# Optimization experiments

Measured on AMD Instinct MI355X. Metric: run time of the kernel, lower is better.

Reference implementation:

```python
import jax, jax.numpy as jnp
import numpy as np

NH = 16            # num_heads
HD = 64            # head_dim
HID = NH * HD      # hidden_size = 1024
MLP = 4 * HID      # mlp_hidden_dim = 4096
B, LI, LT = 1, 2048, 512
EPS = 1e-6


def _ln(x):
    # LayerNorm without affine, eps=1e-6
    mu = jnp.mean(x, -1, keepdims=True)
    var = jnp.mean((x - mu) ** 2, -1, keepdims=True)
    return (x - mu) * jax.lax.rsqrt(var + EPS)


def _rms(x, scale):
    # QK RMSNorm over head_dim with learned scale
    return x * jax.lax.rsqrt(jnp.mean(x * x, -1, keepdims=True) + EPS) * scale


def _modulate(vec, w, b):
    # Modulation(double=True): Linear(silu(vec)) -> 6 chunks, broadcast over seq
    out = jnp.dot(jax.nn.silu(vec), w) + b           # [B, 6*HID]
    return jnp.split(out[:, None, :], 6, axis=-1)


def _qkv(x_mod, qkv_w, q_scale, k_scale):
    b, l, _ = x_mod.shape
    qkv = jnp.dot(x_mod, qkv_w).reshape(b, l, 3, NH, HD)
    qkv = jnp.transpose(qkv, (2, 0, 3, 1, 4))         # [3, B, H, L, D]
    q, k, v = qkv[0], qkv[1], qkv[2]
    return _rms(q, q_scale), _rms(k, k_scale), v


def _attn(q, k, v):
    s = jnp.einsum('bhqd,bhkd->bhqk', q, k) * (HD ** -0.5)
    a = jax.nn.softmax(s, axis=-1)
    o = jnp.einsum('bhqk,bhkd->bhqd', a, v)
    b, h, l, d = o.shape
    return jnp.transpose(o, (0, 2, 1, 3)).reshape(b, l, h * d)  # B L (H D)


def _mlp(x, w1, b1, w2, b2):
    return jnp.dot(jax.nn.gelu(jnp.dot(x, w1) + b1, approximate=True), w2) + b2


def setup_inputs() -> dict:
    key = jax.random.key(0)
    ks = iter(jax.random.split(key, 40))
    def rn(shape, s=1.0):
        return jax.random.normal(next(ks), shape, jnp.float32) * s
    return {
        'img': rn((B, LI, HID)),
        'txt': rn((B, LT, HID)),
        'vec': rn((B, HID)),
        'img_mod_w': rn((HID, 6 * HID), 0.02), 'img_mod_b': jnp.zeros((6 * HID,), jnp.float32),
        'txt_mod_w': rn((HID, 6 * HID), 0.02), 'txt_mod_b': jnp.zeros((6 * HID,), jnp.float32),
        'img_qkv_w': rn((HID, 3 * HID), 0.02),
        'img_q_scale': jnp.ones((HD,), jnp.float32), 'img_k_scale': jnp.ones((HD,), jnp.float32),
        'img_proj_w': rn((HID, HID), 0.02), 'img_proj_b': jnp.zeros((HID,), jnp.float32),
        'img_mlp_w1': rn((HID, MLP), 0.02), 'img_mlp_b1': jnp.zeros((MLP,), jnp.float32),
        'img_mlp_w2': rn((MLP, HID), 0.02), 'img_mlp_b2': jnp.zeros((HID,), jnp.float32),
        'txt_qkv_w': rn((HID, 3 * HID), 0.02),
        'txt_q_scale': jnp.ones((HD,), jnp.float32), 'txt_k_scale': jnp.ones((HD,), jnp.float32),
        'txt_proj_w': rn((HID, HID), 0.02), 'txt_proj_b': jnp.zeros((HID,), jnp.float32),
        'txt_mlp_w1': rn((HID, MLP), 0.02), 'txt_mlp_b1': jnp.zeros((MLP,), jnp.float32),
        'txt_mlp_w2': rn((MLP, HID), 0.02), 'txt_mlp_b2': jnp.zeros((HID,), jnp.float32),
    }


def reference(img, txt, vec,
              img_mod_w, img_mod_b, txt_mod_w, txt_mod_b,
              img_qkv_w, img_q_scale, img_k_scale, img_proj_w, img_proj_b,
              img_mlp_w1, img_mlp_b1, img_mlp_w2, img_mlp_b2,
              txt_qkv_w, txt_q_scale, txt_k_scale, txt_proj_w, txt_proj_b,
              txt_mlp_w1, txt_mlp_b1, txt_mlp_w2, txt_mlp_b2):
    i_sh1, i_sc1, i_g1, i_sh2, i_sc2, i_g2 = _modulate(vec, img_mod_w, img_mod_b)
    t_sh1, t_sc1, t_g1, t_sh2, t_sc2, t_g2 = _modulate(vec, txt_mod_w, txt_mod_b)
    iq, ik, iv = _qkv((1 + i_sc1) * _ln(img) + i_sh1, img_qkv_w, img_q_scale, img_k_scale)
    tq, tk, tv = _qkv((1 + t_sc1) * _ln(txt) + t_sh1, txt_qkv_w, txt_q_scale, txt_k_scale)
    q = jnp.concatenate((tq, iq), axis=2)   # txt tokens first, as in source
    k = jnp.concatenate((tk, ik), axis=2)
    v = jnp.concatenate((tv, iv), axis=2)
    attn = _attn(q, k, v)                    # [B, LT+LI, HID]
    lt = txt.shape[1]
    txt_a, img_a = attn[:, :lt], attn[:, lt:]
    img = img + i_g1 * (jnp.dot(img_a, img_proj_w) + img_proj_b)
    img = img + i_g2 * _mlp((1 + i_sc2) * _ln(img) + i_sh2, img_mlp_w1, img_mlp_b1, img_mlp_w2, img_mlp_b2)
    txt = txt + t_g1 * (jnp.dot(txt_a, txt_proj_w) + txt_proj_b)
    txt = txt + t_g2 * _mlp((1 + t_sc2) * _ln(txt) + t_sh2, txt_mlp_w1, txt_mlp_b1, txt_mlp_w2, txt_mlp_b2)
    return (img, txt)
```

## Files before the change

### kernel.cpp

```cpp
#include <hip/hip_runtime.h>
#include <hip/hip_bf16.h>
#include <stdint.h>


#define NHEAD 16
#define HDIM  64
#define HIDD  1024
#define MLPD  4096
#define L_IMG 2048
#define L_TXT 512
#define L_TOT 2560
#define EPSV  1e-6f
#define LOG2E 1.44269504088896f

typedef __attribute__((ext_vector_type(8))) __bf16 bf16x8;
typedef __attribute__((ext_vector_type(4))) float  f32x4;

__device__ __forceinline__ float u2f(uint16_t u) {
    uint32_t i = (uint32_t)u << 16;
    float f; __builtin_memcpy(&f, &i, 4);
    return f;
}
__device__ __forceinline__ uint16_t f2u(float f) {
    uint32_t i; __builtin_memcpy(&i, &f, 4);
    uint32_t r = (i + 0x7fffu + ((i >> 16) & 1u)) >> 16;
    return (uint16_t)r;
}
__device__ __forceinline__ uint32_t pk2(float a, float b) {
    __hip_bfloat162 h = __float22bfloat162_rn(float2{a, b});
    uint32_t r; __builtin_memcpy(&r, &h, 4);
    return r;
}
__device__ __forceinline__ float gelu_tanh(float x) {
    float x3 = x * x * x;
    float t  = tanhf(0.7978845608028654f * (x + 0.044715f * x3));
    return 0.5f * x * (1.f + t);
}

__global__ __launch_bounds__(256) void transpose_all_kernel(
        const float* __restrict__ i0, const float* __restrict__ i1,
        const float* __restrict__ i2, const float* __restrict__ i3,
        const float* __restrict__ i4, const float* __restrict__ i5,
        const float* __restrict__ i6, const float* __restrict__ i7,
        uint16_t* __restrict__ o0, uint16_t* __restrict__ o1,
        uint16_t* __restrict__ o2, uint16_t* __restrict__ o3,
        uint16_t* __restrict__ o4, uint16_t* __restrict__ o5,
        uint16_t* __restrict__ o6, uint16_t* __restrict__ o7) {
    __shared__ float tile[64][65];
    const int b = blockIdx.x, t = threadIdx.x;
    const float* in; uint16_t* out; int K, N, rel;
    if      (b < 768)  { in = i0; out = o0; K = 1024; N = 3072; rel = b; }
    else if (b < 1536) { in = i1; out = o1; K = 1024; N = 3072; rel = b - 768; }
    else if (b < 1792) { in = i2; out = o2; K = 1024; N = 1024; rel = b - 1536; }
    else if (b < 2048) { in = i3; out = o3; K = 1024; N = 1024; rel = b - 1792; }
    else if (b < 3072) { in = i4; out = o4; K = 1024; N = 4096; rel = b - 2048; }
    else if (b < 4096) { in = i5; out = o5; K = 1024; N = 4096; rel = b - 3072; }
    else if (b < 5120) { in = i6; out = o6; K = 4096; N = 1024; rel = b - 4096; }
    else               { in = i7; out = o7; K = 4096; N = 1024; rel = b - 5120; }
    const int nx = N >> 6;
    const int c0 = (rel % nx) * 64;
    const int r0 = (rel / nx) * 64;
#pragma unroll
    for (int p = 0; p < 4; p++) {
        int row  = p * 16 + (t >> 4);
        int col4 = (t & 15) * 4;
        float4 v = *(const float4*)(in + (size_t)(r0 + row) * N + c0 + col4);
        tile[row][col4 + 0] = v.x; tile[row][col4 + 1] = v.y;
        tile[row][col4 + 2] = v.z; tile[row][col4 + 3] = v.w;
    }
    __syncthreads();
#pragma unroll
    for (int p = 0; p < 4; p++) {
        int row  = p * 16 + (t >> 4);
        int col4 = (t & 15) * 4;
        ushort4 v;
        v.x = f2u(tile[col4 + 0][row]); v.y = f2u(tile[col4 + 1][row]);
        v.z = f2u(tile[col4 + 2][row]); v.w = f2u(tile[col4 + 3][row]);
        *(ushort4*)(out + (size_t)(c0 + row) * K + r0 + col4) = v;
    }
}

__global__ __launch_bounds__(256) void transpose_v_kernel(const uint16_t* __restrict__ Vb,
                                                          uint16_t* __restrict__ Vt) {
    __shared__ uint16_t tile[64][68];
    const int t  = threadIdx.x;
    const int p0 = blockIdx.x * 64;
    const int h  = blockIdx.y;
    const uint16_t* src = Vb + ((size_t)h * L_TOT + p0) * HDIM;
#pragma unroll
    for (int p = 0; p < 4; p++) {
        int row = p * 16 + (t >> 4);
        int c4  = (t & 15) * 4;
        ushort4 v = *(const ushort4*)(src + (size_t)row * HDIM + c4);
        tile[row][c4 + 0] = v.x; tile[row][c4 + 1] = v.y;
        tile[row][c4 + 2] = v.z; tile[row][c4 + 3] = v.w;
    }
    __syncthreads();
    uint16_t* dst = Vt + (size_t)h * HDIM * L_TOT;
#pragma unroll
    for (int p = 0; p < 4; p++) {
        int d  = p * 16 + (t >> 4);
        int c4 = (t & 15) * 4;
        ushort4 v;
        v.x = tile[c4 + 0][d]; v.y = tile[c4 + 1][d];
        v.z = tile[c4 + 2][d]; v.w = tile[c4 + 3][d];
        *(ushort4*)(dst + (size_t)d * L_TOT + p0 + c4) = v;
    }
}

__global__ __launch_bounds__(256) void mod_gemv_kernel(const float* __restrict__ vec,
                                                       const float* __restrict__ w0,
                                                       const float* __restrict__ b0,
                                                       float* __restrict__ m0,
                                                       const float* __restrict__ w1,
                                                       const float* __restrict__ b1,
                                                       float* __restrict__ m1) {
    const float* w   = blockIdx.z ? w1 : w0;
    const float* b   = blockIdx.z ? b1 : b0;
    float*       mod = blockIdx.z ? m1 : m0;
    __shared__ float s[HIDD];
    __shared__ float part[4][64];
    const int t = threadIdx.x;
    for (int i = t; i < HIDD; i += 256) {
        float x = vec[i];
        s[i] = x / (1.f + __expf(-x));
    }
    __syncthreads();
    const int col = blockIdx.x * 64 + (t & 63);
    const int ks  = t >> 6;
    float acc = 0.f;
#pragma unroll 8
    for (int k = ks * 256; k < ks * 256 + 256; k++)
        acc += s[k] * w[(size_t)k * 6144 + col];
    part[ks][t & 63] = acc;
    __syncthreads();
    if (t < 64) {
        float r = part[0][t] + part[1][t] + part[2][t] + part[3][t];
        mod[blockIdx.x * 64 + t] = r + b[blockIdx.x * 64 + t];
    }
}

__global__ __launch_bounds__(256) void ln_mod_kernel(const float* __restrict__ xi,
                                                     const float* __restrict__ xt,
                                                     const float* __restrict__ mi,
                                                     const float* __restrict__ mt_,
                                                     int scOff, int shOff,
                                                     uint16_t* __restrict__ oi,
                                                     uint16_t* __restrict__ ot) {
    __shared__ float red[8];
    int row = blockIdx.x;
    const float* x; const float* mod; uint16_t* xm;
    if (row < L_IMG) { x = xi; mod = mi; xm = oi; }
    else             { x = xt; mod = mt_; xm = ot; row -= L_IMG; }
    const int t = threadIdx.x;
    const size_t base = (size_t)row * HIDD + t * 4;
    float4 u = *(const float4*)(x + base);
    float v[4] = {u.x, u.y, u.z, u.w};
    float s = v[0] + v[1] + v[2] + v[3];
    float q = v[0]*v[0] + v[1]*v[1] + v[2]*v[2] + v[3]*v[3];
#pragma unroll
    for (int o = 32; o; o >>= 1) { s += __shfl_down(s, o); q += __shfl_down(q, o); }
    if ((t & 63) == 0) { red[t >> 6] = s; red[4 + (t >> 6)] = q; }
    __syncthreads();
    s = red[0] + red[1] + red[2] + red[3];
    q = red[4] + red[5] + red[6] + red[7];
    const float mu  = s * (1.f / HIDD);
    const float var = q * (1.f / HIDD) - mu * mu;
    const float rs  = rsqrtf(var + EPSV);
    ushort4 o;
    {
        int col = t * 4;
        float y0 = (v[0] - mu) * rs, y1 = (v[1] - mu) * rs;
        float y2 = (v[2] - mu) * rs, y3 = (v[3] - mu) * rs;
        o.x = f2u(y0 + mod[scOff + col + 0] * y0 + mod[shOff + col + 0]);
        o.y = f2u(y1 + mod[scOff + col + 1] * y1 + mod[shOff + col + 1]);
        o.z = f2u(y2 + mod[scOff + col + 2] * y2 + mod[shOff + col + 2]);
        o.w = f2u(y3 + mod[scOff + col + 3] * y3 + mod[shOff + col + 3]);
    }
    *(ushort4*)(xm + base) = o;
}

template <int EPI>
__global__ __launch_bounds__(256, 2) void gemm_kernel(
        const uint16_t* __restrict__ A0, const uint16_t* __restrict__ A1,
        const uint16_t* __restrict__ B0, const uint16_t* __restrict__ B1,
        int M0, int M1, int N, int K,
        const float* __restrict__ bias0, const float* __restrict__ bias1,
        const float* __restrict__ gate0, const float* __restrict__ gate1,
        const float* __restrict__ resid0, const float* __restrict__ resid1,
        void* __restrict__ C0, void* __restrict__ C1) {
    const int z = blockIdx.z;
    const int M = z ? M1 : M0;
    const int m0 = blockIdx.y * 128;
    if (m0 >= M) return;
    const uint16_t* A     = z ? A1 : A0;
    const uint16_t* BT    = z ? B1 : B0;
    const float*    bias  = z ? bias1 : bias0;
    const float*    gate  = z ? gate1 : gate0;
    const float*    resid = z ? resid1 : resid0;
    void*           C     = z ? C1 : C0;

    __shared__ uint16_t As[2][128 * 32];
    __shared__ uint16_t Bs[2][128 * 32];
    const int t = threadIdx.x;
    const int w = t >> 6, l = t & 63;
    const int lr = l & 15, lg = l >> 4;
    const int n0 = blockIdx.x * 128;
    const int srow = l >> 2, scol = (l & 3) * 8;
    const int c0 = w * 2;
    const int wr = (w >> 1) * 64, wc = (w & 1) * 64;

    auto stage = [&](int buf, int kt) {
#pragma unroll
        for (int i = 0; i < 2; i++) {
            const int c = c0 + i;
            const uint16_t* ga = A  + (size_t)(m0 + c * 16 + srow) * K + kt + scol;
            const uint16_t* gb = BT + (size_t)(n0 + c * 16 + srow) * K + kt + scol;
            __builtin_amdgcn_global_load_lds(
                (__attribute__((address_space(1))) void*)ga,
                (__attribute__((address_space(3))) void*)(As[buf] + c * 512), 16, 0, 0);
            __builtin_amdgcn_global_load_lds(
                (__attribute__((address_space(1))) void*)gb,
                (__attribute__((address_space(3))) void*)(Bs[buf] + c * 512), 16, 0, 0);
        }
    };

    const f32x4 z4 = {0.f, 0.f, 0.f, 0.f};
    f32x4 acc[4][4];
#pragma unroll
    for (int i = 0; i < 4; i++)
#pragma unroll
        for (int j = 0; j < 4; j++) acc[i][j] = z4;

    stage(0, 0);
    int cur = 0;
    for (int kt = 0; kt < K; kt += 32) {
        __syncthreads();
        if (kt + 32 < K) stage(cur ^ 1, kt + 32);
        bf16x8 af[4], bfr[4];
#pragma unroll
        for (int mi = 0; mi < 4; mi++)
            af[mi] = *(const bf16x8*)(As[cur] + (wr + mi * 16 + lr) * 32 + lg * 8);
#pragma unroll
        for (int nj = 0; nj < 4; nj++)
            bfr[nj] = *(const bf16x8*)(Bs[cur] + (wc + nj * 16 + lr) * 32 + lg * 8);
#pragma unroll
        for (int mi = 0; mi < 4; mi++)
#pragma unroll
            for (int nj = 0; nj < 4; nj++)
                acc[mi][nj] = __builtin_amdgcn_mfma_f32_16x16x32_bf16(
                    af[mi], bfr[nj], acc[mi][nj], 0, 0, 0);
        cur ^= 1;
    }

#pragma unroll
    for (int mi = 0; mi < 4; mi++)
#pragma unroll
        for (int nj = 0; nj < 4; nj++) {
            const int col = n0 + wc + nj * 16 + lr;
            float bv = 0.f, gv = 0.f;
            if (EPI != 0) bv = bias[col];
            if (EPI == 2) gv = gate[col];
#pragma unroll
            for (int j = 0; j < 4; j++) {
                const int row = m0 + wr + mi * 16 + lg * 4 + j;
                const size_t idx = (size_t)row * N + col;
                float v = acc[mi][nj][j];
                if (EPI == 0) {
                    ((uint16_t*)C)[idx] = f2u(v);
                } else if (EPI == 1) {
                    ((uint16_t*)C)[idx] = f2u(gelu_tanh(v + bv));
                } else {
                    ((float*)C)[idx] = resid[idx] + gv * (v + bv);
                }
            }
        }
}

__global__ __launch_bounds__(256, 2) void gemm_splitk_kernel(
        const uint16_t* __restrict__ A0, const uint16_t* __restrict__ A1,
        const uint16_t* __restrict__ B0, const uint16_t* __restrict__ B1,
        int M0, int M1, int N, int K, int KS,
        float* __restrict__ P0, float* __restrict__ P1) {
    const int z = blockIdx.z & 1;
    const int split = blockIdx.z >> 1;
    const int M = z ? M1 : M0;
    const int m0 = blockIdx.y * 128;
    if (m0 >= M) return;
    const uint16_t* A  = z ? A1 : A0;
    const uint16_t* BT = z ? B1 : B0;
    float* P = (z ? P1 : P0) + (size_t)split * M * N;

    __shared__ uint16_t As[2][128 * 32];
    __shared__ uint16_t Bs[2][128 * 32];
    const int t = threadIdx.x;
    const int w = t >> 6, l = t & 63;
    const int lr = l & 15, lg = l >> 4;
    const int n0 = blockIdx.x * 128;
    const int srow = l >> 2, scol = (l & 3) * 8;
    const int c0 = w * 2;
    const int wr = (w >> 1) * 64, wc = (w & 1) * 64;

    auto stage = [&](int buf, int kt) {
#pragma unroll
        for (int i = 0; i < 2; i++) {
            const int c = c0 + i;
            const uint16_t* ga = A  + (size_t)(m0 + c * 16 + srow) * K + kt + scol;
            const uint16_t* gb = BT + (size_t)(n0 + c * 16 + srow) * K + kt + scol;
            __builtin_amdgcn_global_load_lds(
                (__attribute__((address_space(1))) void*)ga,
                (__attribute__((address_space(3))) void*)(As[buf] + c * 512), 16, 0, 0);
            __builtin_amdgcn_global_load_lds(
                (__attribute__((address_space(1))) void*)gb,
                (__attribute__((address_space(3))) void*)(Bs[buf] + c * 512), 16, 0, 0);
        }
    };

    const f32x4 z4 = {0.f, 0.f, 0.f, 0.f};
    f32x4 acc[4][4];
#pragma unroll
    for (int i = 0; i < 4; i++)
#pragma unroll
        for (int j = 0; j < 4; j++) acc[i][j] = z4;

    const int kbeg = split * KS, kend = kbeg + KS;
    stage(0, kbeg);
    int cur = 0;
    for (int kt = kbeg; kt < kend; kt += 32) {
        __syncthreads();
        if (kt + 32 < kend) stage(cur ^ 1, kt + 32);
        bf16x8 af[4], bfr[4];
#pragma unroll
        for (int mi = 0; mi < 4; mi++)
            af[mi] = *(const bf16x8*)(As[cur] + (wr + mi * 16 + lr) * 32 + lg * 8);
#pragma unroll
        for (int nj = 0; nj < 4; nj++)
            bfr[nj] = *(const bf16x8*)(Bs[cur] + (wc + nj * 16 + lr) * 32 + lg * 8);
#pragma unroll
        for (int mi = 0; mi < 4; mi++)
#pragma unroll
            for (int nj = 0; nj < 4; nj++)
                acc[mi][nj] = __builtin_amdgcn_mfma_f32_16x16x32_bf16(
                    af[mi], bfr[nj], acc[mi][nj], 0, 0, 0);
        cur ^= 1;
    }

#pragma unroll
    for (int mi = 0; mi < 4; mi++)
#pragma unroll
        for (int nj = 0; nj < 4; nj++) {
            const int col = n0 + wc + nj * 16 + lr;
#pragma unroll
            for (int j = 0; j < 4; j++) {
                const int row = m0 + wr + mi * 16 + lg * 4 + j;
                P[(size_t)row * N + col] = acc[mi][nj][j];
            }
        }
}

template <int NS>
__global__ __launch_bounds__(256) void splitk_reduce_kernel(
        const float* __restrict__ P0, const float* __restrict__ P1,
        const float* __restrict__ bias0, const float* __restrict__ bias1,
        const float* __restrict__ gate0, const float* __restrict__ gate1,
        const float* __restrict__ resid0, const float* __restrict__ resid1,
        float* __restrict__ O0, float* __restrict__ O1, int M0, int M1) {
    const int z = blockIdx.z;
    const float* P     = z ? P1 : P0;
    const float* bias  = z ? bias1 : bias0;
    const float* gate  = z ? gate1 : gate0;
    const float* resid = z ? resid1 : resid0;
    float*       O     = z ? O1 : O0;
    const int M = z ? M1 : M0;
    const size_t MN = (size_t)M * HIDD;
    const size_t nvec = MN / 4;
    for (size_t i = blockIdx.x * 256 + threadIdx.x; i < nvec; i += (size_t)gridDim.x * 256) {
        const size_t e = i * 4;
        const int col = (int)(e & (HIDD - 1));
        float4 bi = *(const float4*)(bias + col);
        float sx = bi.x, sy = bi.y, sz = bi.z, sw = bi.w;
#pragma unroll
        for (int sp = 0; sp < NS; sp++) {
            float4 a = *(const float4*)(P + (size_t)sp * MN + e);
            sx += a.x; sy += a.y; sz += a.z; sw += a.w;
        }
        float4 r = *(const float4*)(resid + e);
        float4 g = *(const float4*)(gate + col);
        float4 o;
        o.x = r.x + g.x * sx;
        o.y = r.y + g.y * sy;
        o.z = r.z + g.z * sz;
        o.w = r.w + g.w * sw;
        *(float4*)(O + e) = o;
    }
}

__global__ __launch_bounds__(256) void rms_scatter_kernel(
        const uint16_t* __restrict__ qkvi, const uint16_t* __restrict__ qkvt,
        const float* __restrict__ iqs, const float* __restrict__ iks,
        const float* __restrict__ tqs, const float* __restrict__ tks,
        uint16_t* __restrict__ Q, uint16_t* __restrict__ Kb, uint16_t* __restrict__ V) {
    const int p = blockIdx.x;
    const uint16_t* base;
    const float* qs; const float* ks;
    if (p < L_TXT) { base = qkvt + (size_t)p * 3072;            qs = tqs; ks = tks; }
    else           { base = qkvi + (size_t)(p - L_TXT) * 3072;  qs = iqs; ks = iks; }
    const int t = threadIdx.x;
    const int head = t >> 4, d0 = (t & 15) * 4;
    const size_t obase = ((size_t)head * L_TOT + p) * HDIM + d0;
    {
        ushort4 u = *(const ushort4*)(base + head * HDIM + d0);
        float v0 = u2f(u.x), v1 = u2f(u.y), v2 = u2f(u.z), v3 = u2f(u.w);
        float ss = v0*v0 + v1*v1 + v2*v2 + v3*v3;
        ss += __shfl_xor(ss, 1); ss += __shfl_xor(ss, 2);
        ss += __shfl_xor(ss, 4); ss += __shfl_xor(ss, 8);
        float inv = rsqrtf(ss * (1.f / HDIM) + EPSV) * (0.125f * LOG2E);
        ushort4 o;
        o.x = f2u(v0 * inv * qs[d0 + 0]);
        o.y = f2u(v1 * inv * qs[d0 + 1]);
        o.z = f2u(v2 * inv * qs[d0 + 2]);
        o.w = f2u(v3 * inv * qs[d0 + 3]);
        *(ushort4*)(Q + obase) = o;
    }
    {
        ushort4 u = *(const ushort4*)(base + HIDD + head * HDIM + d0);
        float v0 = u2f(u.x), v1 = u2f(u.y), v2 = u2f(u.z), v3 = u2f(u.w);
        float ss = v0*v0 + v1*v1 + v2*v2 + v3*v3;
        ss += __shfl_xor(ss, 1); ss += __shfl_xor(ss, 2);
        ss += __shfl_xor(ss, 4); ss += __shfl_xor(ss, 8);
        float inv = rsqrtf(ss * (1.f / HDIM) + EPSV);
        ushort4 o;
        o.x = f2u(v0 * inv * ks[d0 + 0]);
        o.y = f2u(v1 * inv * ks[d0 + 1]);
        o.z = f2u(v2 * inv * ks[d0 + 2]);
        o.w = f2u(v3 * inv * ks[d0 + 3]);
        *(ushort4*)(Kb + obase) = o;
    }
    {
        ushort4 u = *(const ushort4*)(base + 2 * HIDD + head * HDIM + d0);
        *(ushort4*)(V + obase) = u;
    }
}

__global__ __launch_bounds__(256, 4) void attn_kernel(const uint16_t* __restrict__ Q,
                                                      const uint16_t* __restrict__ Kg,
                                                      const uint16_t* __restrict__ Vt,
                                                      uint16_t* __restrict__ Opart,
                                                      float* __restrict__ lbuf) {
    __shared__ __align__(16) uint16_t Ks[64 * 64];
    __shared__ __align__(16) uint16_t Vs[64 * 64];
    __shared__ __align__(16) uint16_t Pl[4][16][72];
    const int t = threadIdx.x;
    const int w = t >> 6, l = t & 63;
    const int lr = l & 15, lg = l >> 4;
    const int h = blockIdx.y;
    const int s = blockIdx.z;
    const int q0 = blockIdx.x * 64 + w * 16;
    const uint16_t* Qh = Q  + (size_t)h * L_TOT * HDIM;
    const uint16_t* Kh = Kg + (size_t)h * L_TOT * HDIM;
    const uint16_t* Vh = Vt + (size_t)h * HDIM * L_TOT;

    const bf16x8 qf0 = *(const bf16x8*)(Qh + (size_t)(q0 + lr) * HDIM + lg * 8);
    const bf16x8 qf1 = *(const bf16x8*)(Qh + (size_t)(q0 + lr) * HDIM + 32 + lg * 8);

    const int rl = l >> 3;
    const int ce = ((l & 7) ^ rl) * 8;
    const int r0 = w * 16 + rl;
    const int r1 = r0 + 8;
    const int sw = lr & 7;

    const f32x4 z4 = {0.f, 0.f, 0.f, 0.f};
    f32x4 of[4] = {z4, z4, z4, z4};
    float lsum = 0.f;

    const int kbeg = s * (L_TOT / 2);
    const uint16_t* kS0 = Kh + (size_t)(kbeg + r0) * HDIM + ce;
    const uint16_t* kS1 = Kh + (size_t)(kbeg + r1) * HDIM + ce;
    const uint16_t* vS0 = Vh + (size_t)r0 * L_TOT + kbeg + ce;
    const uint16_t* vS1 = Vh + (size_t)r1 * L_TOT + kbeg + ce;

    for (int it = 0; it < (L_TOT / 2) / 64; ++it) {
        __syncthreads();
        __builtin_amdgcn_global_load_lds(
            (__attribute__((address_space(1))) void*)kS0,
            (__attribute__((address_space(3))) void*)(Ks + w * 1024), 16, 0, 0);
        __builtin_amdgcn_global_load_lds(
            (__attribute__((address_space(1))) void*)kS1,
            (__attribute__((address_space(3))) void*)(Ks + w * 1024 + 512), 16, 0, 0);
        __builtin_amdgcn_global_load_lds(
            (__attribute__((address_space(1))) void*)vS0,
            (__attribute__((address_space(3))) void*)(Vs + w * 1024), 16, 0, 0);
        __builtin_amdgcn_global_load_lds(
            (__attribute__((address_space(1))) void*)vS1,
            (__attribute__((address_space(3))) void*)(Vs + w * 1024 + 512), 16, 0, 0);
        kS0 += (size_t)64 * HDIM; kS1 += (size_t)64 * HDIM;
        vS0 += 64; vS1 += 64;
        __syncthreads();
        f32x4 sf[4] = {z4, z4, z4, z4};
#pragma unroll
        for (int kb = 0; kb < 4; kb++) {
            bf16x8 a0 = *(const bf16x8*)(Ks + (kb * 16 + lr) * 64 + ((lg ^ sw) * 8));
            bf16x8 a1 = *(const bf16x8*)(Ks + (kb * 16 + lr) * 64 + (((4 + lg) ^ sw) * 8));
            sf[kb] = __builtin_amdgcn_mfma_f32_16x16x32_bf16(a0, qf0, sf[kb], 0, 0, 0);
            sf[kb] = __builtin_amdgcn_mfma_f32_16x16x32_bf16(a1, qf1, sf[kb], 0, 0, 0);
        }
        uint32_t pw[8];
        float rs = 0.f;
#pragma unroll
        for (int kb = 0; kb < 4; kb++) {
            float p0 = exp2f(sf[kb][0]);
            float p1 = exp2f(sf[kb][1]);
            float p2 = exp2f(sf[kb][2]);
            float p3 = exp2f(sf[kb][3]);
            rs += (p0 + p1) + (p2 + p3);
            pw[kb * 2]     = pk2(p0, p1);
            pw[kb * 2 + 1] = pk2(p2, p3);
        }
        lsum += rs;
#pragma unroll
        for (int kb = 0; kb < 4; kb++) {
            uint2 u = {pw[kb * 2], pw[kb * 2 + 1]};
            *(uint2*)&Pl[w][lr][kb * 16 + lg * 4] = u;
        }
        bf16x8 pb0 = *(const bf16x8*)&Pl[w][lr][lg * 8];
        bf16x8 pb1 = *(const bf16x8*)&Pl[w][lr][32 + lg * 8];
#pragma unroll
        for (int dj = 0; dj < 4; dj++) {
            bf16x8 v0 = *(const bf16x8*)(Vs + (dj * 16 + lr) * 64 + ((lg ^ sw) * 8));
            bf16x8 v1 = *(const bf16x8*)(Vs + (dj * 16 + lr) * 64 + (((4 + lg) ^ sw) * 8));
            of[dj] = __builtin_amdgcn_mfma_f32_16x16x32_bf16(v0, pb0, of[dj], 0, 0, 0);
            of[dj] = __builtin_amdgcn_mfma_f32_16x16x32_bf16(v1, pb1, of[dj], 0, 0, 0);
        }
    }
    lsum += __shfl_xor(lsum, 16);
    lsum += __shfl_xor(lsum, 32);
    const float inv = 1.f / lsum;
    const int row = q0 + lr;
    const size_t ob = ((size_t)(s * NHEAD + h) * L_TOT + row) * HDIM;
#pragma unroll
    for (int dj = 0; dj < 4; dj++) {
        uint2 u;
        u.x = pk2(of[dj][0] * inv, of[dj][1] * inv);
        u.y = pk2(of[dj][2] * inv, of[dj][3] * inv);
        *(uint2*)(Opart + ob + dj * 16 + lg * 4) = u;
    }
    if (lg == 0) lbuf[(size_t)(s * NHEAD + h) * L_TOT + row] = lsum;
}

__global__ __launch_bounds__(256) void attn_merge_kernel(const uint16_t* __restrict__ Opart,
                                                         const float* __restrict__ lbuf,
                                                         uint16_t* __restrict__ attn) {
    const int t = threadIdx.x;
    const int row = blockIdx.x * 16 + (t >> 4);
    const int h = blockIdx.y;
    const int d = (t & 15) * 4;
    const size_t i0 = (size_t)(0 * NHEAD + h) * L_TOT + row;
    const size_t i1 = (size_t)(1 * NHEAD + h) * L_TOT + row;
    float l0 = lbuf[i0], l1 = lbuf[i1];
    float inv = 1.f / (l0 + l1);
    float w0 = l0 * inv, w1 = l1 * inv;
    ushort4 a = *(const ushort4*)(Opart + i0 * HDIM + d);
    ushort4 b = *(const ushort4*)(Opart + i1 * HDIM + d);
    ushort4 o;
    o.x = f2u(u2f(a.x) * w0 + u2f(b.x) * w1);
    o.y = f2u(u2f(a.y) * w0 + u2f(b.y) * w1);
    o.z = f2u(u2f(a.z) * w0 + u2f(b.z) * w1);
    o.w = f2u(u2f(a.w) * w0 + u2f(b.w) * w1);
    *(ushort4*)(attn + (size_t)row * HIDD + h * HDIM + d) = o;
}

extern "C" void kernel_launch(void* const* d_in, const int* in_sizes, int n_in,
                              void* d_out, int out_size, void* d_ws, size_t ws_size,
                              hipStream_t stream) {
    const float* img        = (const float*)d_in[0];
    const float* txt        = (const float*)d_in[1];
    const float* vec        = (const float*)d_in[2];
    const float* img_mod_w  = (const float*)d_in[3];
    const float* img_mod_b  = (const float*)d_in[4];
    const float* txt_mod_w  = (const float*)d_in[5];
    const float* txt_mod_b  = (const float*)d_in[6];
    const float* img_qkv_w  = (const float*)d_in[7];
    const float* img_q_s    = (const float*)d_in[8];
    const float* img_k_s    = (const float*)d_in[9];
    const float* img_proj_w = (const float*)d_in[10];
    const float* img_proj_b = (const float*)d_in[11];
    const float* img_mlp_w1 = (const float*)d_in[12];
    const float* img_mlp_b1 = (const float*)d_in[13];
    const float* img_mlp_w2 = (const float*)d_in[14];
    const float* img_mlp_b2 = (const float*)d_in[15];
    const float* txt_qkv_w  = (const float*)d_in[16];
    const float* txt_q_s    = (const float*)d_in[17];
    const float* txt_k_s    = (const float*)d_in[18];
    const float* txt_proj_w = (const float*)d_in[19];
    const float* txt_proj_b = (const float*)d_in[20];
    const float* txt_mlp_w1 = (const float*)d_in[21];
    const float* txt_mlp_b1 = (const float*)d_in[22];
    const float* txt_mlp_w2 = (const float*)d_in[23];
    const float* txt_mlp_b2 = (const float*)d_in[24];

    float* out_img = (float*)d_out;
    float* out_txt = out_img + (size_t)L_IMG * HIDD;

    char* ws = (char*)d_ws;
    size_t off = 0;
    auto alloc = [&](size_t bytes) -> void* {
        void* p = ws + off;
        off += bytes;
        off = (off + 255) & ~(size_t)255;
        return p;
    };
    uint16_t* wtQKVi = (uint16_t*)alloc((size_t)3072 * 1024 * 2);
    uint16_t* wtQKVt = (uint16_t*)alloc((size_t)3072 * 1024 * 2);
    uint16_t* wtPRJi = (uint16_t*)alloc((size_t)1024 * 1024 * 2);
    uint16_t* wtPRJt = (uint16_t*)alloc((size_t)1024 * 1024 * 2);
    uint16_t* wtM1i  = (uint16_t*)alloc((size_t)4096 * 1024 * 2);
    uint16_t* wtM1t  = (uint16_t*)alloc((size_t)4096 * 1024 * 2);
    uint16_t* wtM2i  = (uint16_t*)alloc((size_t)1024 * 4096 * 2);
    uint16_t* wtM2t  = (uint16_t*)alloc((size_t)1024 * 4096 * 2);
    float*    modi   = (float*)alloc(6144 * 4);
    float*    modt   = (float*)alloc(6144 * 4);
    uint16_t* xm1i   = (uint16_t*)alloc((size_t)L_IMG * HIDD * 2);
    uint16_t* xm1t   = (uint16_t*)alloc((size_t)L_TXT * HIDD * 2);
    uint16_t* qkvi   = (uint16_t*)alloc((size_t)L_IMG * 3072 * 2);
    uint16_t* qkvt   = (uint16_t*)alloc((size_t)L_TXT * 3072 * 2);
    uint16_t* Qb     = (uint16_t*)alloc((size_t)NHEAD * L_TOT * HDIM * 2);
    uint16_t* Kb     = (uint16_t*)alloc((size_t)NHEAD * L_TOT * HDIM * 2);
    uint16_t* Vb     = (uint16_t*)alloc((size_t)NHEAD * L_TOT * HDIM * 2);
    uint16_t* Vtb    = (uint16_t*)alloc((size_t)NHEAD * L_TOT * HDIM * 2);
    uint16_t* attn   = (uint16_t*)alloc((size_t)L_TOT * HIDD * 2);
    float*    x2i    = (float*)alloc((size_t)L_IMG * HIDD * 4);
    float*    x2t    = (float*)alloc((size_t)L_TXT * HIDD * 4);
    uint16_t* xm2i   = (uint16_t*)alloc((size_t)L_IMG * HIDD * 2);
    uint16_t* xm2t   = (uint16_t*)alloc((size_t)L_TXT * HIDD * 2);
    uint16_t* hi     = (uint16_t*)alloc((size_t)L_IMG * MLPD * 2);
    uint16_t* ht     = (uint16_t*)alloc((size_t)L_TXT * MLPD * 2);
    uint16_t* Opart  = qkvi;
    float*    lbuf   = (float*)qkvt;
    float*    pPJi   = (float*)Qb;
    float*    pPJt   = pPJi + (size_t)2 * L_IMG * HIDD;
    float*    pM2i   = (float*)xm1i;
    float*    pM2t   = pM2i + (size_t)4 * L_IMG * HIDD;
    (void)ws_size; (void)in_sizes; (void)n_in; (void)out_size;

    transpose_all_kernel<<<6144, 256, 0, stream>>>(
        img_qkv_w, txt_qkv_w, img_proj_w, txt_proj_w,
        img_mlp_w1, txt_mlp_w1, img_mlp_w2, txt_mlp_w2,
        wtQKVi, wtQKVt, wtPRJi, wtPRJt, wtM1i, wtM1t, wtM2i, wtM2t);

    mod_gemv_kernel<<<dim3(96, 1, 2), 256, 0, stream>>>(
        vec, img_mod_w, img_mod_b, modi, txt_mod_w, txt_mod_b, modt);

    ln_mod_kernel<<<L_IMG + L_TXT, 256, 0, stream>>>(img, txt, modi, modt, 1024, 0, xm1i, xm1t);

    gemm_kernel<0><<<dim3(3072 / 128, L_IMG / 128, 2), 256, 0, stream>>>(
        xm1i, xm1t, wtQKVi, wtQKVt, L_IMG, L_TXT, 3072, 1024,
        nullptr, nullptr, nullptr, nullptr, nullptr, nullptr, qkvi, qkvt);

    rms_scatter_kernel<<<L_TOT, 256, 0, stream>>>(
        qkvi, qkvt, img_q_s, img_k_s, txt_q_s, txt_k_s, Qb, Kb, Vb);

    transpose_v_kernel<<<dim3(L_TOT / 64, NHEAD), 256, 0, stream>>>(Vb, Vtb);

    attn_kernel<<<dim3(L_TOT / 64, NHEAD, 2), 256, 0, stream>>>(Qb, Kb, Vtb, Opart, lbuf);
    attn_merge_kernel<<<dim3(L_TOT / 16, NHEAD), 256, 0, stream>>>(Opart, lbuf, attn);

    gemm_splitk_kernel<<<dim3(1024 / 128, L_IMG / 128, 4), 256, 0, stream>>>(
        attn + (size_t)L_TXT * HIDD, attn, wtPRJi, wtPRJt, L_IMG, L_TXT, 1024, 1024, 512,
        pPJi, pPJt);
    splitk_reduce_kernel<2><<<dim3(512, 1, 2), 256, 0, stream>>>(
        pPJi, pPJt, img_proj_b, txt_proj_b, modi + 2048, modt + 2048,
        img, txt, x2i, x2t, L_IMG, L_TXT);

    ln_mod_kernel<<<L_IMG + L_TXT, 256, 0, stream>>>(x2i, x2t, modi, modt, 4096, 3072, xm2i, xm2t);

    gemm_kernel<1><<<dim3(MLPD / 128, L_IMG / 128, 2), 256, 0, stream>>>(
        xm2i, xm2t, wtM1i, wtM1t, L_IMG, L_TXT, MLPD, 1024,
        img_mlp_b1, txt_mlp_b1, nullptr, nullptr, nullptr, nullptr, hi, ht);

    gemm_splitk_kernel<<<dim3(1024 / 128, L_IMG / 128, 8), 256, 0, stream>>>(
        hi, ht, wtM2i, wtM2t, L_IMG, L_TXT, 1024, MLPD, MLPD / 4, pM2i, pM2t);
    splitk_reduce_kernel<4><<<dim3(512, 1, 2), 256, 0, stream>>>(
        pM2i, pM2t, img_mlp_b2, txt_mlp_b2, modi + 5120, modt + 5120,
        x2i, x2t, out_img, out_txt, L_IMG, L_TXT);
}
```

Measured before the change: 278.8 us.

## Double-buffer K/V tiles in attention kernel to overlap loads with MFMA

Gives the attention kernel two LDS buffers each for K and V. The next tile's global-to-LDS async load is issued right after the barrier, while MFMA work runs on the current tile, which also drops one barrier per iteration. The aim is to hide global memory latency behind compute. In exchange, LDS use per block roughly doubles for K/V, and the launch bound drops from 4 to 3 blocks per CU, which may cut occupancy.

```diff
diff --git a/kernel.cpp b/kernel.cpp
--- a/kernel.cpp
+++ b/kernel.cpp
@@ -442,13 +442,13 @@
     }
 }
 
-__global__ __launch_bounds__(256, 4) void attn_kernel(const uint16_t* __restrict__ Q,
+__global__ __launch_bounds__(256, 3) void attn_kernel(const uint16_t* __restrict__ Q,
                                                       const uint16_t* __restrict__ Kg,
                                                       const uint16_t* __restrict__ Vt,
                                                       uint16_t* __restrict__ Opart,
                                                       float* __restrict__ lbuf) {
-    __shared__ __align__(16) uint16_t Ks[64 * 64];
-    __shared__ __align__(16) uint16_t Vs[64 * 64];
+    __shared__ __align__(16) uint16_t Ks[2][64 * 64];
+    __shared__ __align__(16) uint16_t Vs[2][64 * 64];
     __shared__ __align__(16) uint16_t Pl[4][16][72];
     const int t = threadIdx.x;
     const int w = t >> 6, l = t & 63;
@@ -469,38 +469,44 @@
     const int r1 = r0 + 8;
     const int sw = lr & 7;
 
-    const f32x4 z4 = {0.f, 0.f, 0.f, 0.f};
-    f32x4 of[4] = {z4, z4, z4, z4};
-    float lsum = 0.f;
-
     const int kbeg = s * (L_TOT / 2);
     const uint16_t* kS0 = Kh + (size_t)(kbeg + r0) * HDIM + ce;
     const uint16_t* kS1 = Kh + (size_t)(kbeg + r1) * HDIM + ce;
     const uint16_t* vS0 = Vh + (size_t)r0 * L_TOT + kbeg + ce;
     const uint16_t* vS1 = Vh + (size_t)r1 * L_TOT + kbeg + ce;
 
-    for (int it = 0; it < (L_TOT / 2) / 64; ++it) {
+    auto stage = [&](int buf, int it) {
+        const size_t ko = (size_t)it * 64 * HDIM;
+        const size_t vo = (size_t)it * 64;
+        __builtin_amdgcn_global_load_lds(
+            (__attribute__((address_space(1))) void*)(kS0 + ko),
+            (__attribute__((address_space(3))) void*)(Ks[buf] + w * 1024), 16, 0, 0);
+        __builtin_amdgcn_global_load_lds(
+            (__attribute__((address_space(1))) void*)(kS1 + ko),
+            (__attribute__((address_space(3))) void*)(Ks[buf] + w * 1024 + 512), 16, 0, 0);
+        __builtin_amdgcn_global_load_lds(
+            (__attribute__((address_space(1))) void*)(vS0 + vo),
+            (__attribute__((address_space(3))) void*)(Vs[buf] + w * 1024), 16, 0, 0);
+        __builtin_amdgcn_global_load_lds(
+            (__attribute__((address_space(1))) void*)(vS1 + vo),
+            (__attribute__((address_space(3))) void*)(Vs[buf] + w * 1024 + 512), 16, 0, 0);
+    };
+
+    const f32x4 z4 = {0.f, 0.f, 0.f, 0.f};
+    f32x4 of[4] = {z4, z4, z4, z4};
+    float lsum = 0.f;
+
+    const int NIT = (L_TOT / 2) / 64;
+    stage(0, 0);
+    int cur = 0;
+    for (int it = 0; it < NIT; ++it) {
         __syncthreads();
-        __builtin_amdgcn_global_load_lds(
-            (__attribute__((address_space(1))) void*)kS0,
-            (__attribute__((address_space(3))) void*)(Ks + w * 1024), 16, 0, 0);
-        __builtin_amdgcn_global_load_lds(
-            (__attribute__((address_space(1))) void*)kS1,
-            (__attribute__((address_space(3))) void*)(Ks + w * 1024 + 512), 16, 0, 0);
-        __builtin_amdgcn_global_load_lds(
-            (__attribute__((address_space(1))) void*)vS0,
-            (__attribute__((address_space(3))) void*)(Vs + w * 1024), 16, 0, 0);
-        __builtin_amdgcn_global_load_lds(
-            (__attribute__((address_space(1))) void*)vS1,
-            (__attribute__((address_space(3))) void*)(Vs + w * 1024 + 512), 16, 0, 0);
-        kS0 += (size_t)64 * HDIM; kS1 += (size_t)64 * HDIM;
-        vS0 += 64; vS1 += 64;
-        __syncthreads();
+        if (it + 1 < NIT) stage(cur ^ 1, it + 1);
         f32x4 sf[4] = {z4, z4, z4, z4};
 #pragma unroll
         for (int kb = 0; kb < 4; kb++) {
-            bf16x8 a0 = *(const bf16x8*)(Ks + (kb * 16 + lr) * 64 + ((lg ^ sw) * 8));
-            bf16x8 a1 = *(const bf16x8*)(Ks + (kb * 16 + lr) * 64 + (((4 + lg) ^ sw) * 8));
+            bf16x8 a0 = *(const bf16x8*)(Ks[cur] + (kb * 16 + lr) * 64 + ((lg ^ sw) * 8));
+            bf16x8 a1 = *(const bf16x8*)(Ks[cur] + (kb * 16 + lr) * 64 + (((4 + lg) ^ sw) * 8));
             sf[kb] = __builtin_amdgcn_mfma_f32_16x16x32_bf16(a0, qf0, sf[kb], 0, 0, 0);
             sf[kb] = __builtin_amdgcn_mfma_f32_16x16x32_bf16(a1, qf1, sf[kb], 0, 0, 0);
         }
@@ -526,11 +532,12 @@
         bf16x8 pb1 = *(const bf16x8*)&Pl[w][lr][32 + lg * 8];
 #pragma unroll
         for (int dj = 0; dj < 4; dj++) {
-            bf16x8 v0 = *(const bf16x8*)(Vs + (dj * 16 + lr) * 64 + ((lg ^ sw) * 8));
-            bf16x8 v1 = *(const bf16x8*)(Vs + (dj * 16 + lr) * 64 + (((4 + lg) ^ sw) * 8));
+            bf16x8 v0 = *(const bf16x8*)(Vs[cur] + (dj * 16 + lr) * 64 + ((lg ^ sw) * 8));
+            bf16x8 v1 = *(const bf16x8*)(Vs[cur] + (dj * 16 + lr) * 64 + (((4 + lg) ^ sw) * 8));
             of[dj] = __builtin_amdgcn_mfma_f32_16x16x32_bf16(v0, pb0, of[dj], 0, 0, 0);
             of[dj] = __builtin_amdgcn_mfma_f32_16x16x32_bf16(v1, pb1, of[dj], 0, 0, 0);
         }
+        cur ^= 1;
     }
     lsum += __shfl_xor(lsum, 16);
     lsum += __shfl_xor(lsum, 32);
```

Measured after the change: 282.5 us. No clear change (+1.4%).

## Add XCD-aware block swizzle to GEMMs and halve MLP2 split-K factor

Applied to the files above, without the earlier changes.

Adds an XCD swizzle that remaps the linear block index so consecutive tiles land on the same XCD, aiming to improve L2 reuse of A/B tiles in both GEMM kernels. The second MLP GEMM changes from split-K 4 to split-K 2, which halves the fp32 partial-sum traffic and reduce work but leaves fewer blocks and longer K loops per block. The partial buffers for the proj and MLP2 split-K are merged into one shared scratch region.

```diff
diff --git a/kernel.cpp b/kernel.cpp
--- a/kernel.cpp
+++ b/kernel.cpp
@@ -35,6 +35,16 @@
     float x3 = x * x * x;
     float t  = tanhf(0.7978845608028654f * (x + 0.044715f * x3));
     return 0.5f * x * (1.f + t);
+}
+__device__ __forceinline__ void xcd_swizzle(int& bx, int& by) {
+    const int nxg = gridDim.x, nyg = gridDim.y;
+    const int nwg = nxg * nyg;
+    int lin = by * nxg + bx;
+    if ((nwg & 7) == 0) {
+        lin = (lin & 7) * (nwg >> 3) + (lin >> 3);
+        bx = lin % nxg;
+        by = lin / nxg;
+    }
 }
 
 __global__ __launch_bounds__(256) void transpose_all_kernel(
@@ -189,9 +199,11 @@
         const float* __restrict__ gate0, const float* __restrict__ gate1,
         const float* __restrict__ resid0, const float* __restrict__ resid1,
         void* __restrict__ C0, void* __restrict__ C1) {
+    int bx = blockIdx.x, by = blockIdx.y;
+    xcd_swizzle(bx, by);
     const int z = blockIdx.z;
     const int M = z ? M1 : M0;
-    const int m0 = blockIdx.y * 128;
+    const int m0 = by * 128;
     if (m0 >= M) return;
     const uint16_t* A     = z ? A1 : A0;
     const uint16_t* BT    = z ? B1 : B0;
@@ -205,7 +217,7 @@
     const int t = threadIdx.x;
     const int w = t >> 6, l = t & 63;
     const int lr = l & 15, lg = l >> 4;
-    const int n0 = blockIdx.x * 128;
+    const int n0 = bx * 128;
     const int srow = l >> 2, scol = (l & 3) * 8;
     const int c0 = w * 2;
     const int wr = (w >> 1) * 64, wc = (w & 1) * 64;
@@ -282,10 +294,12 @@
         const uint16_t* __restrict__ B0, const uint16_t* __restrict__ B1,
         int M0, int M1, int N, int K, int KS,
         float* __restrict__ P0, float* __restrict__ P1) {
+    int bx = blockIdx.x, by = blockIdx.y;
+    xcd_swizzle(bx, by);
     const int z = blockIdx.z & 1;
     const int split = blockIdx.z >> 1;
     const int M = z ? M1 : M0;
-    const int m0 = blockIdx.y * 128;
+    const int m0 = by * 128;
     if (m0 >= M) return;
     const uint16_t* A  = z ? A1 : A0;
     const uint16_t* BT = z ? B1 : B0;
@@ -296,7 +310,7 @@
     const int t = threadIdx.x;
     const int w = t >> 6, l = t & 63;
     const int lr = l & 15, lg = l >> 4;
-    const int n0 = blockIdx.x * 128;
+    const int n0 = bx * 128;
     const int srow = l >> 2, scol = (l & 3) * 8;
     const int c0 = w * 2;
     const int wr = (w >> 1) * 64, wc = (w & 1) * 64;
@@ -636,10 +650,8 @@
     uint16_t* ht     = (uint16_t*)alloc((size_t)L_TXT * MLPD * 2);
     uint16_t* Opart  = qkvi;
     float*    lbuf   = (float*)qkvt;
-    float*    pPJi   = (float*)Qb;
-    float*    pPJt   = pPJi + (size_t)2 * L_IMG * HIDD;
-    float*    pM2i   = (float*)xm1i;
-    float*    pM2t   = pM2i + (size_t)4 * L_IMG * HIDD;
+    float*    pSKi   = (float*)Qb;
+    float*    pSKt   = pSKi + (size_t)2 * L_IMG * HIDD;
     (void)ws_size; (void)in_sizes; (void)n_in; (void)out_size;
 
     transpose_all_kernel<<<6144, 256, 0, stream>>>(
@@ -666,9 +678,9 @@
 
     gemm_splitk_kernel<<<dim3(1024 / 128, L_IMG / 128, 4), 256, 0, stream>>>(
         attn + (size_t)L_TXT * HIDD, attn, wtPRJi, wtPRJt, L_IMG, L_TXT, 1024, 1024, 512,
-        pPJi, pPJt);
+        pSKi, pSKt);
     splitk_reduce_kernel<2><<<dim3(512, 1, 2), 256, 0, stream>>>(
-        pPJi, pPJt, img_proj_b, txt_proj_b, modi + 2048, modt + 2048,
+        pSKi, pSKt, img_proj_b, txt_proj_b, modi + 2048, modt + 2048,
         img, txt, x2i, x2t, L_IMG, L_TXT);
 
     ln_mod_kernel<<<L_IMG + L_TXT, 256, 0, stream>>>(x2i, x2t, modi, modt, 4096, 3072, xm2i, xm2t);
@@ -677,9 +689,9 @@
         xm2i, xm2t, wtM1i, wtM1t, L_IMG, L_TXT, MLPD, 1024,
         img_mlp_b1, txt_mlp_b1, nullptr, nullptr, nullptr, nullptr, hi, ht);
 
-    gemm_splitk_kernel<<<dim3(1024 / 128, L_IMG / 128, 8), 256, 0, stream>>>(
-        hi, ht, wtM2i, wtM2t, L_IMG, L_TXT, 1024, MLPD, MLPD / 4, pM2i, pM2t);
-    splitk_reduce_kernel<4><<<dim3(512, 1, 2), 256, 0, stream>>>(
-        pM2i, pM2t, img_mlp_b2, txt_mlp_b2, modi + 5120, modt + 5120,
+    gemm_splitk_kernel<<<dim3(1024 / 128, L_IMG / 128, 4), 256, 0, stream>>>(
+        hi, ht, wtM2i, wtM2t, L_IMG, L_TXT, 1024, MLPD, MLPD / 2, pSKi, pSKt);
+    splitk_reduce_kernel<2><<<dim3(512, 1, 2), 256, 0, stream>>>(
+        pSKi, pSKt, img_mlp_b2, txt_mlp_b2, modi + 5120, modt + 5120,
         x2i, x2t, out_img, out_txt, L_IMG, L_TXT);
 }
```

Measured after the change: 296.2 us. +6.3%, slower.

## Fuse V transpose into RMS scatter and halve MLP down-proj split-K

Applied to the files above, without the earlier changes.

Merges the separate V transpose kernel into the QK RMS-norm scatter kernel: each block now handles a 64-token tile for one head, normalises Q/K, and writes V already transposed through shared memory. This removes one launch and the intermediate V buffer round trip. The MLP second GEMM's split-K factor drops from 4 to 2, which halves the partial-sum traffic and reduction work but gives the GEMM fewer blocks to run in parallel. Partial buffers are reassigned to reuse the xm1i region.

```diff
diff --git a/kernel.cpp b/kernel.cpp
--- a/kernel.cpp
+++ b/kernel.cpp
@@ -80,34 +80,6 @@
     }
 }
 
-__global__ __launch_bounds__(256) void transpose_v_kernel(const uint16_t* __restrict__ Vb,
-                                                          uint16_t* __restrict__ Vt) {
-    __shared__ uint16_t tile[64][68];
-    const int t  = threadIdx.x;
-    const int p0 = blockIdx.x * 64;
-    const int h  = blockIdx.y;
-    const uint16_t* src = Vb + ((size_t)h * L_TOT + p0) * HDIM;
-#pragma unroll
-    for (int p = 0; p < 4; p++) {
-        int row = p * 16 + (t >> 4);
-        int c4  = (t & 15) * 4;
-        ushort4 v = *(const ushort4*)(src + (size_t)row * HDIM + c4);
-        tile[row][c4 + 0] = v.x; tile[row][c4 + 1] = v.y;
-        tile[row][c4 + 2] = v.z; tile[row][c4 + 3] = v.w;
-    }
-    __syncthreads();
-    uint16_t* dst = Vt + (size_t)h * HDIM * L_TOT;
-#pragma unroll
-    for (int p = 0; p < 4; p++) {
-        int d  = p * 16 + (t >> 4);
-        int c4 = (t & 15) * 4;
-        ushort4 v;
-        v.x = tile[c4 + 0][d]; v.y = tile[c4 + 1][d];
-        v.z = tile[c4 + 2][d]; v.w = tile[c4 + 3][d];
-        *(ushort4*)(dst + (size_t)d * L_TOT + p0 + c4) = v;
-    }
-}
-
 __global__ __launch_bounds__(256) void mod_gemv_kernel(const float* __restrict__ vec,
                                                        const float* __restrict__ w0,
                                                        const float* __restrict__ b0,
@@ -399,46 +371,84 @@
         const uint16_t* __restrict__ qkvi, const uint16_t* __restrict__ qkvt,
         const float* __restrict__ iqs, const float* __restrict__ iks,
         const float* __restrict__ tqs, const float* __restrict__ tks,
-        uint16_t* __restrict__ Q, uint16_t* __restrict__ Kb, uint16_t* __restrict__ V) {
-    const int p = blockIdx.x;
-    const uint16_t* base;
-    const float* qs; const float* ks;
+        uint16_t* __restrict__ Q, uint16_t* __restrict__ Kb, uint16_t* __restrict__ Vt) {
+    __shared__ uint16_t tile[64][68];
+    const int t = threadIdx.x;
+    const int ptile = blockIdx.x * 64;
+    const int h = blockIdx.y;
+    const int pl = t >> 2;
+    const int d0 = (t & 3) * 16;
+    const int p = ptile + pl;
+    const uint16_t* base; const float* qs; const float* ks;
     if (p < L_TXT) { base = qkvt + (size_t)p * 3072;            qs = tqs; ks = tks; }
     else           { base = qkvi + (size_t)(p - L_TXT) * 3072;  qs = iqs; ks = iks; }
-    const int t = threadIdx.x;
-    const int head = t >> 4, d0 = (t & 15) * 4;
-    const size_t obase = ((size_t)head * L_TOT + p) * HDIM + d0;
+
     {
-        ushort4 u = *(const ushort4*)(base + head * HDIM + d0);
-        float v0 = u2f(u.x), v1 = u2f(u.y), v2 = u2f(u.z), v3 = u2f(u.w);
-        float ss = v0*v0 + v1*v1 + v2*v2 + v3*v3;
+        const uint16_t* src = base + h * HDIM + d0;
+        float v[16];
+#pragma unroll
+        for (int i = 0; i < 4; i++) {
+            ushort4 u = *(const ushort4*)(src + i * 4);
+            v[i*4+0] = u2f(u.x); v[i*4+1] = u2f(u.y);
+            v[i*4+2] = u2f(u.z); v[i*4+3] = u2f(u.w);
+        }
+        float ss = 0.f;
+#pragma unroll
+        for (int i = 0; i < 16; i++) ss += v[i] * v[i];
         ss += __shfl_xor(ss, 1); ss += __shfl_xor(ss, 2);
-        ss += __shfl_xor(ss, 4); ss += __shfl_xor(ss, 8);
         float inv = rsqrtf(ss * (1.f / HDIM) + EPSV) * (0.125f * LOG2E);
-        ushort4 o;
-        o.x = f2u(v0 * inv * qs[d0 + 0]);
-        o.y = f2u(v1 * inv * qs[d0 + 1]);
-        o.z = f2u(v2 * inv * qs[d0 + 2]);
-        o.w = f2u(v3 * inv * qs[d0 + 3]);
-        *(ushort4*)(Q + obase) = o;
+        uint16_t* dq = Q + ((size_t)h * L_TOT + p) * HDIM + d0;
+#pragma unroll
+        for (int i = 0; i < 4; i++) {
+            ushort4 o;
+            o.x = f2u(v[i*4+0] * inv * qs[d0 + i*4 + 0]);
+            o.y = f2u(v[i*4+1] * inv * qs[d0 + i*4 + 1]);
+            o.z = f2u(v[i*4+2] * inv * qs[d0 + i*4 + 2]);
+            o.w = f2u(v[i*4+3] * inv * qs[d0 + i*4 + 3]);
+            *(ushort4*)(dq + i * 4) = o;
+        }
     }
     {
-        ushort4 u = *(const ushort4*)(base + HIDD + head * HDIM + d0);
-        float v0 = u2f(u.x), v1 = u2f(u.y), v2 = u2f(u.z), v3 = u2f(u.w);
-        float ss = v0*v0 + v1*v1 + v2*v2 + v3*v3;
+        const uint16_t* src = base + HIDD + h * HDIM + d0;
+        float v[16];
+#pragma unroll
+        for (int i = 0; i < 4; i++) {
+            ushort4 u = *(const ushort4*)(src + i * 4);
+            v[i*4+0] = u2f(u.x); v[i*4+1] = u2f(u.y);
+            v[i*4+2] = u2f(u.z); v[i*4+3] = u2f(u.w);
+        }
+        float ss = 0.f;
+#pragma unroll
+        for (int i = 0; i < 16; i++) ss += v[i] * v[i];
         ss += __shfl_xor(ss, 1); ss += __shfl_xor(ss, 2);
-        ss += __shfl_xor(ss, 4); ss += __shfl_xor(ss, 8);
         float inv = rsqrtf(ss * (1.f / HDIM) + EPSV);
-        ushort4 o;
-        o.x = f2u(v0 * inv * ks[d0 + 0]);
-        o.y = f2u(v1 * inv * ks[d0 + 1]);
-        o.z = f2u(v2 * inv * ks[d0 + 2]);
-        o.w = f2u(v3 * inv * ks[d0 + 3]);
-        *(ushort4*)(Kb + obase) = o;
+        uint16_t* dk = Kb + ((size_t)h * L_TOT + p) * HDIM + d0;
+#pragma unroll
+        for (int i = 0; i < 4; i++) {
+            ushort4 o;
+            o.x = f2u(v[i*4+0] * inv * ks[d0 + i*4 + 0]);
+            o.y = f2u(v[i*4+1] * inv * ks[d0 + i*4 + 1]);
+            o.z = f2u(v[i*4+2] * inv * ks[d0 + i*4 + 2]);
+            o.w = f2u(v[i*4+3] * inv * ks[d0 + i*4 + 3]);
+            *(ushort4*)(dk + i * 4) = o;
+        }
     }
     {
-        ushort4 u = *(const ushort4*)(base + 2 * HIDD + head * HDIM + d0);
-        *(ushort4*)(V + obase) = u;
+        const uint16_t* src = base + 2 * HIDD + h * HDIM + d0;
+#pragma unroll
+        for (int i = 0; i < 4; i++)
+            *(ushort4*)&tile[pl][d0 + i * 4] = *(const ushort4*)(src + i * 4);
+    }
+    __syncthreads();
+    uint16_t* dst = Vt + (size_t)h * HDIM * L_TOT;
+#pragma unroll
+    for (int pp = 0; pp < 4; pp++) {
+        int d  = pp * 16 + (t >> 4);
+        int c4 = (t & 15) * 4;
+        ushort4 v;
+        v.x = tile[c4 + 0][d]; v.y = tile[c4 + 1][d];
+        v.z = tile[c4 + 2][d]; v.w = tile[c4 + 3][d];
+        *(ushort4*)(dst + (size_t)d * L_TOT + ptile + c4) = v;
     }
 }
 
@@ -625,7 +635,6 @@
     uint16_t* qkvt   = (uint16_t*)alloc((size_t)L_TXT * 3072 * 2);
     uint16_t* Qb     = (uint16_t*)alloc((size_t)NHEAD * L_TOT * HDIM * 2);
     uint16_t* Kb     = (uint16_t*)alloc((size_t)NHEAD * L_TOT * HDIM * 2);
-    uint16_t* Vb     = (uint16_t*)alloc((size_t)NHEAD * L_TOT * HDIM * 2);
     uint16_t* Vtb    = (uint16_t*)alloc((size_t)NHEAD * L_TOT * HDIM * 2);
     uint16_t* attn   = (uint16_t*)alloc((size_t)L_TOT * HIDD * 2);
     float*    x2i    = (float*)alloc((size_t)L_IMG * HIDD * 4);
@@ -636,10 +645,8 @@
     uint16_t* ht     = (uint16_t*)alloc((size_t)L_TXT * MLPD * 2);
     uint16_t* Opart  = qkvi;
     float*    lbuf   = (float*)qkvt;
-    float*    pPJi   = (float*)Qb;
-    float*    pPJt   = pPJi + (size_t)2 * L_IMG * HIDD;
-    float*    pM2i   = (float*)xm1i;
-    float*    pM2t   = pM2i + (size_t)4 * L_IMG * HIDD;
+    float*    pSKi   = (float*)xm1i;
+    float*    pSKt   = pSKi + (size_t)2 * L_IMG * HIDD;
     (void)ws_size; (void)in_sizes; (void)n_in; (void)out_size;
 
     transpose_all_kernel<<<6144, 256, 0, stream>>>(
@@ -656,19 +663,17 @@
         xm1i, xm1t, wtQKVi, wtQKVt, L_IMG, L_TXT, 3072, 1024,
         nullptr, nullptr, nullptr, nullptr, nullptr, nullptr, qkvi, qkvt);
 
-    rms_scatter_kernel<<<L_TOT, 256, 0, stream>>>(
-        qkvi, qkvt, img_q_s, img_k_s, txt_q_s, txt_k_s, Qb, Kb, Vb);
-
-    transpose_v_kernel<<<dim3(L_TOT / 64, NHEAD), 256, 0, stream>>>(Vb, Vtb);
+    rms_scatter_kernel<<<dim3(L_TOT / 64, NHEAD), 256, 0, stream>>>(
+        qkvi, qkvt, img_q_s, img_k_s, txt_q_s, txt_k_s, Qb, Kb, Vtb);
 
     attn_kernel<<<dim3(L_TOT / 64, NHEAD, 2), 256, 0, stream>>>(Qb, Kb, Vtb, Opart, lbuf);
     attn_merge_kernel<<<dim3(L_TOT / 16, NHEAD), 256, 0, stream>>>(Opart, lbuf, attn);
 
     gemm_splitk_kernel<<<dim3(1024 / 128, L_IMG / 128, 4), 256, 0, stream>>>(
         attn + (size_t)L_TXT * HIDD, attn, wtPRJi, wtPRJt, L_IMG, L_TXT, 1024, 1024, 512,
-        pPJi, pPJt);
+        pSKi, pSKt);
     splitk_reduce_kernel<2><<<dim3(512, 1, 2), 256, 0, stream>>>(
-        pPJi, pPJt, img_proj_b, txt_proj_b, modi + 2048, modt + 2048,
+        pSKi, pSKt, img_proj_b, txt_proj_b, modi + 2048, modt + 2048,
         img, txt, x2i, x2t, L_IMG, L_TXT);
 
     ln_mod_kernel<<<L_IMG + L_TXT, 256, 0, stream>>>(x2i, x2t, modi, modt, 4096, 3072, xm2i, xm2t);
@@ -677,9 +682,9 @@
         xm2i, xm2t, wtM1i, wtM1t, L_IMG, L_TXT, MLPD, 1024,
         img_mlp_b1, txt_mlp_b1, nullptr, nullptr, nullptr, nullptr, hi, ht);
 
-    gemm_splitk_kernel<<<dim3(1024 / 128, L_IMG / 128, 8), 256, 0, stream>>>(
-        hi, ht, wtM2i, wtM2t, L_IMG, L_TXT, 1024, MLPD, MLPD / 4, pM2i, pM2t);
-    splitk_reduce_kernel<4><<<dim3(512, 1, 2), 256, 0, stream>>>(
-        pM2i, pM2t, img_mlp_b2, txt_mlp_b2, modi + 5120, modt + 5120,
+    gemm_splitk_kernel<<<dim3(1024 / 128, L_IMG / 128, 4), 256, 0, stream>>>(
+        hi, ht, wtM2i, wtM2t, L_IMG, L_TXT, 1024, MLPD, MLPD / 2, pSKi, pSKt);
+    splitk_reduce_kernel<2><<<dim3(512, 1, 2), 256, 0, stream>>>(
+        pSKi, pSKt, img_mlp_b2, txt_mlp_b2, modi + 5120, modt + 5120,
         x2i, x2t, out_img, out_txt, L_IMG, L_TXT);
 }
```

Result: no change. 273.9 us (-1.7%).
